# Kernel optimization log

Measured on AMD Instinct MI355X. Metric: run time of the kernel, lower is better.

The kernel has to match this reference:

```python
import jax, jax.numpy as jnp
import numpy as np

B, T, D, H = 32, 512, 512, 8
DH = D // H  # 64


def _pos_enc(t, d):
    # pos / 10000^(2i/d) for ALL i, then sin on even cols, cos on odd cols, scaled by sqrt(d)
    pos = np.arange(t, dtype=np.float64)[:, None]
    i = np.arange(d, dtype=np.float64)[None, :]
    ang = pos / np.power(10000.0, 2.0 * i / d)
    pe = np.empty((t, d), dtype=np.float64)
    pe[:, 0::2] = np.sin(ang[:, 0::2])
    pe[:, 1::2] = np.cos(ang[:, 1::2])
    return jnp.asarray(pe * np.sqrt(float(d)), dtype=jnp.float32)


def setup_inputs() -> dict:
    key = jax.random.key(0)
    ks = jax.random.split(key, 9)
    return {
        "queries": jax.random.normal(ks[0], (B, T, D), dtype=jnp.float32),
        "keys": jax.random.normal(ks[1], (B, T, D), dtype=jnp.float32),
        "query_masks": jax.random.randint(ks[2], (B,), 0, T, dtype=jnp.int32),
        "key_masks": jax.random.randint(ks[3], (B,), 0, T, dtype=jnp.int32),
        "W_Q": jax.random.normal(ks[4], (D, D), dtype=jnp.float32) * 0.05,
        "W_K": jax.random.normal(ks[5], (D, D), dtype=jnp.float32) * 0.05,
        "W_V": jax.random.normal(ks[6], (D, D), dtype=jnp.float32) * 0.05,
        "fw1": jax.random.normal(ks[7], (D, 4 * D), dtype=jnp.float32) * 0.05,
        "fw2": jax.random.normal(ks[8], (4 * D, D), dtype=jnp.float32) * 0.05,
    }


def reference(queries, keys, query_masks, key_masks, W_Q, W_K, W_V, fw1, fw2):
    pe = _pos_enc(T, D)  # [T, D]
    # Source bug kept: queries = posenc(queries); keys = posenc(queries)  -> keys input unused
    q1 = queries + pe[None]          # [B,T,D]
    k1 = q1 + pe[None]               # pos-encoded twice
    Q = q1 @ W_Q                     # [B,T,D]
    Kp = k1 @ W_K                    # [B,T,D]
    V = Kp @ W_V                     # source bug kept: values from projected keys
    # split heads (head-major fold in the original concat(split) idiom)
    Qh = Q.reshape(B, T, H, DH).transpose(2, 0, 1, 3)   # [H,B,T,dh]
    Kh = Kp.reshape(B, T, H, DH).transpose(2, 0, 1, 3)
    Vh = V.reshape(B, T, H, DH).transpose(2, 0, 1, 3)
    scores = jnp.einsum('hbqd,hbkd->hbqk', Qh, Kh) / jnp.sqrt(jnp.float32(DH))
    # source subtracts max over the QUERY axis (axis=1 of [H*B,T,T]) = axis 2 here
    scores = scores - scores.max(axis=2, keepdims=True)
    attn = jax.nn.softmax(scores, axis=-1)
    qmask = (jnp.arange(T)[None, :] < query_masks[:, None]).astype(jnp.float32)  # [B,T]
    attn = attn * qmask[None, :, :, None]
    out = jnp.einsum('hbqk,hbkd->hbqd', attn, Vh)       # [H,B,T,dh]
    result = out.transpose(1, 2, 0, 3).reshape(B, T, D) + q1  # residual with pos-encoded queries
    hidden = jax.nn.relu(result @ fw1)                  # [B,T,4D]
    result = result + hidden @ fw2                      # residual; no layer norm (use_layer_norm=False)
    return result
```

## Files before the change

### kernel.cpp

```cpp
#include <hip/hip_runtime.h>
#include <cstdint>
#include <cstddef>

typedef __bf16 bf16x8 __attribute__((ext_vector_type(8)));
typedef float f32x4 __attribute__((ext_vector_type(4)));
using u16 = unsigned short;
using u32 = unsigned int;

__device__ __forceinline__ u16 f2b(float f) {
  u32 u = __float_as_uint(f);
  u32 r = u + 0x7FFFu + ((u >> 16) & 1u);
  return (u16)(r >> 16);
}
__device__ __forceinline__ float b2f(u16 h) { return __uint_as_float((u32)h << 16); }

__device__ __forceinline__ void gload16(const void* g, void* l) {
  __builtin_amdgcn_global_load_lds((const __attribute__((address_space(1))) void*)g,
                                   (__attribute__((address_space(3))) void*)l, 16, 0, 0);
}

__device__ __forceinline__ u32 mapf(float f) {
  u32 u = __float_as_uint(f);
  return (u & 0x80000000u) ? ~u : (u | 0x80000000u);
}
__device__ __forceinline__ float unmapf(u32 k) {
  u32 u = (k & 0x80000000u) ? (k ^ 0x80000000u) : ~k;
  return __uint_as_float(u);
}
__device__ __forceinline__ u32 cvtpk(float lo, float hi) {
  u32 r;
  asm("v_cvt_pk_bf16_f32 %0, %1, %2" : "=v"(r) : "v"(lo), "v"(hi));
  return r;
}

__device__ __forceinline__ void xcd_swizzle(int& bx, int& by) {
  const int gx = gridDim.x;
  const int nwg = gx * gridDim.y;
  int n = blockIdx.y * gx + blockIdx.x;
  const int cpx = nwg >> 3;
  n = (n & 7) * cpx + (n >> 3);
  bx = n % gx;
  by = n / gx;
}

#define MFMA __builtin_amdgcn_mfma_f32_16x16x32_bf16

__global__ void pe_kernel(float* __restrict__ pe) {
  int i = blockIdx.x * 256 + threadIdx.x;
  if (i >= 512 * 512) return;
  int t = i >> 9, d = i & 511;
  double ang = (double)t * exp((double)d * (-2.0 / 512.0) * log(10000.0));
  double v = (d & 1) ? cos(ang) : sin(ang);
  pe[i] = (float)(v * 22.627416997969522);
}

__global__ void wconv_kernel(const float* __restrict__ WQ, const float* __restrict__ WK,
                             const float* __restrict__ WV, const float* __restrict__ f1,
                             const float* __restrict__ f2,
                             u16* __restrict__ WQth, u16* __restrict__ WQtl,
                             u16* __restrict__ WKth, u16* __restrict__ WKtl,
                             u16* __restrict__ WKb, u16* __restrict__ WVt,
                             u16* __restrict__ f1t, u16* __restrict__ f2t) {
  int i = blockIdx.x * 256 + threadIdx.x;
  if (i < 262144) {
    int n = i >> 9, k = i & 511;
    float wq = WQ[k * 512 + n];
    u16 h = f2b(wq);
    WQth[i] = h;
    WQtl[i] = f2b(wq - b2f(h));
    float wk = WK[k * 512 + n];
    h = f2b(wk);
    WKth[i] = h;
    WKtl[i] = f2b(wk - b2f(h));
    WKb[i] = f2b(WK[i]);
    WVt[i] = f2b(WV[k * 512 + n]);
  } else if (i < 262144 + 1048576) {
    int i2 = i - 262144;
    int n = i2 >> 9, k = i2 & 511;
    f1t[i2] = f2b(f1[k * 2048 + n]);
  } else if (i < 262144 + 2097152) {
    int i3 = i - 262144 - 1048576;
    int n = i3 >> 11, k = i3 & 2047;
    f2t[i3] = f2b(f2[k * 512 + n]);
  }
}

__global__ void prep_kernel(const float* __restrict__ q, const float* __restrict__ pe,
                            u16* __restrict__ q1h, u16* __restrict__ q1l,
                            u16* __restrict__ k1h, u16* __restrict__ k1l) {
  int i4 = blockIdx.x * 256 + threadIdx.x;
  if (i4 >= 2097152) return;
  int i = i4 * 4;
  int td = i & (262144 - 1);
  float4 qv = *(const float4*)&q[i];
  float4 pv = *(const float4*)&pe[td];
  float q1[4] = {qv.x + pv.x, qv.y + pv.y, qv.z + pv.z, qv.w + pv.w};
  float pp[4] = {pv.x, pv.y, pv.z, pv.w};
  ushort4 qh4, ql4, kh4, kl4;
  u16* qhp = (u16*)&qh4;
  u16* qlp = (u16*)&ql4;
  u16* khp = (u16*)&kh4;
  u16* klp = (u16*)&kl4;
#pragma unroll
  for (int j = 0; j < 4; ++j) {
    float k1 = q1[j] + pp[j];
    u16 h = f2b(q1[j]);
    qhp[j] = h;
    qlp[j] = f2b(q1[j] - b2f(h));
    h = f2b(k1);
    khp[j] = h;
    klp[j] = f2b(k1 - b2f(h));
  }
  *(ushort4*)&q1h[i] = qh4;
  *(ushort4*)&q1l[i] = ql4;
  *(ushort4*)&k1h[i] = kh4;
  *(ushort4*)&k1l[i] = kl4;
}

#define GM_BF16 0
#define GM_RELU 2
#define GM_ADDF32 3

template <int MODE>
__global__ __launch_bounds__(256, 3) void gemm_bt(const u16* __restrict__ A,
                                                  const u16* __restrict__ B, int M, int N, int K,
                                                  u16* __restrict__ outb, float* __restrict__ outf,
                                                  const float* __restrict__ res) {
  __shared__ u16 As[128 * 32];
  __shared__ u16 Bs[128 * 32];
  int bxi, byi;
  xcd_swizzle(bxi, byi);
  const int tid = threadIdx.x, lane = tid & 63, w = tid >> 6;
  const int wm = w >> 1, wn = w & 1;
  const long aBase = (long)bxi * 128;
  const long bBase = (long)byi * 128;
  f32x4 acc[4][4] = {};
  const int nk = K >> 5;
  for (int kt = 0; kt < nk; ++kt) {
#pragma unroll
    for (int i = 0; i < 2; ++i) {
      const int c = w * 2 + i;
      const int off = c * 1024 + lane * 16;
      const int r = off >> 6, cb = off & 63;
      gload16((const char*)A + ((aBase + r) * (long)K + (long)kt * 32) * 2 + cb,
              (char*)As + c * 1024);
      gload16((const char*)B + ((bBase + r) * (long)K + (long)kt * 32) * 2 + cb,
              (char*)Bs + c * 1024);
    }
    __syncthreads();
    bf16x8 af[4], bfr[4];
#pragma unroll
    for (int x = 0; x < 4; ++x) {
      af[x] = *(const bf16x8*)&As[(wm * 64 + x * 16 + (lane & 15)) * 32 + (lane >> 4) * 8];
      bfr[x] = *(const bf16x8*)&Bs[(wn * 64 + x * 16 + (lane & 15)) * 32 + (lane >> 4) * 8];
    }
#pragma unroll
    for (int mf = 0; mf < 4; ++mf)
#pragma unroll
      for (int nf = 0; nf < 4; ++nf)
        acc[mf][nf] = MFMA(af[mf], bfr[nf], acc[mf][nf], 0, 0, 0);
    __syncthreads();
  }
#pragma unroll
  for (int mf = 0; mf < 4; ++mf)
#pragma unroll
    for (int nf = 0; nf < 4; ++nf) {
      const long row0 = aBase + wm * 64 + mf * 16 + (lane >> 4) * 4;
      const long col = bBase + wn * 64 + nf * 16 + (lane & 15);
#pragma unroll
      for (int j = 0; j < 4; ++j) {
        float v = acc[mf][nf][j];
        const long row = row0 + j;
        if constexpr (MODE == GM_BF16)
          outb[row * N + col] = f2b(v);
        else if constexpr (MODE == GM_RELU)
          outb[row * N + col] = f2b(v > 0.f ? v : 0.f);
        else
          outf[row * N + col] = res[row * N + col] + v;
      }
    }
}

__global__ __launch_bounds__(256, 3) void gemm_split(const u16* __restrict__ Ah,
                                                     const u16* __restrict__ Al,
                                                     const u16* __restrict__ Bh,
                                                     const u16* __restrict__ Bl, int M, int N,
                                                     int K, u16* __restrict__ Oh,
                                                     u16* __restrict__ Ol) {
  __shared__ u16 Ash[4096], Asl[4096], Bsh[4096], Bsl[4096];
  int bxi, byi;
  xcd_swizzle(bxi, byi);
  const int tid = threadIdx.x, lane = tid & 63, w = tid >> 6;
  const int wm = w >> 1, wn = w & 1;
  const long aBase = (long)bxi * 128;
  const long bBase = (long)byi * 128;
  f32x4 acc[4][4] = {};
  const int nk = K >> 5;
  for (int kt = 0; kt < nk; ++kt) {
#pragma unroll
    for (int i = 0; i < 2; ++i) {
      const int c = w * 2 + i;
      const int off = c * 1024 + lane * 16;
      const int r = off >> 6, cb = off & 63;
      long ga = ((aBase + r) * (long)K + (long)kt * 32) * 2 + cb;
      long gb = ((bBase + r) * (long)K + (long)kt * 32) * 2 + cb;
      gload16((const char*)Ah + ga, (char*)Ash + c * 1024);
      gload16((const char*)Al + ga, (char*)Asl + c * 1024);
      gload16((const char*)Bh + gb, (char*)Bsh + c * 1024);
      gload16((const char*)Bl + gb, (char*)Bsl + c * 1024);
    }
    __syncthreads();
    bf16x8 ah[4], al[4], bh[4], bl[4];
#pragma unroll
    for (int x = 0; x < 4; ++x) {
      int ao = (wm * 64 + x * 16 + (lane & 15)) * 32 + (lane >> 4) * 8;
      int bo = (wn * 64 + x * 16 + (lane & 15)) * 32 + (lane >> 4) * 8;
      ah[x] = *(const bf16x8*)&Ash[ao];
      al[x] = *(const bf16x8*)&Asl[ao];
      bh[x] = *(const bf16x8*)&Bsh[bo];
      bl[x] = *(const bf16x8*)&Bsl[bo];
    }
#pragma unroll
    for (int mf = 0; mf < 4; ++mf)
#pragma unroll
      for (int nf = 0; nf < 4; ++nf) {
        acc[mf][nf] = MFMA(ah[mf], bh[nf], acc[mf][nf], 0, 0, 0);
        acc[mf][nf] = MFMA(ah[mf], bl[nf], acc[mf][nf], 0, 0, 0);
        acc[mf][nf] = MFMA(al[mf], bh[nf], acc[mf][nf], 0, 0, 0);
      }
    __syncthreads();
  }
#pragma unroll
  for (int mf = 0; mf < 4; ++mf)
#pragma unroll
    for (int nf = 0; nf < 4; ++nf) {
      const long row0 = aBase + wm * 64 + mf * 16 + (lane >> 4) * 4;
      const long col = bBase + wn * 64 + nf * 16 + (lane & 15);
#pragma unroll
      for (int j = 0; j < 4; ++j) {
        float v = acc[mf][nf][j];
        const long row = row0 + j;
        u16 h = f2b(v);
        Oh[row * N + col] = h;
        Ol[row * N + col] = f2b(v - b2f(h));
      }
    }
}

__global__ __launch_bounds__(512) void attn_fused(
    const u16* __restrict__ Qh, const u16* __restrict__ Ql, const u16* __restrict__ Kh,
    const u16* __restrict__ Kl, const u16* __restrict__ Vt, const int* __restrict__ qmask,
    const u16* __restrict__ r1h, const u16* __restrict__ r1l, float* __restrict__ resf,
    u16* __restrict__ resb) {
  extern __shared__ char smem[];
  u16* Khi = (u16*)smem;
  u16* Klo = (u16*)(smem + 65536);
  u32* mloc = (u32*)(smem + 131072);
  float* mksf = (float*)(smem + 131072);
  const int tid = threadIdx.x, lane = tid & 63, w = tid >> 6;
  const int qll = lane & 15, g = lane >> 4;
  const int hb = blockIdx.x, b = hb >> 3, h = hb & 7;
  const int qm = qmask[b];
  mloc[tid] = 0u;
  const int srccb = 16 * ((lane & 7) ^ ((lane >> 3) & 7));
#pragma unroll
  for (int c = 0; c < 8; ++c) {
    long gb = ((long)(b * 512 + c * 64 + w * 8 + (lane >> 3)) * 512 + h * 64) * 2 + srccb;
    gload16((const char*)Kh + gb, (char*)Khi + c * 8192 + w * 1024);
    gload16((const char*)Kl + gb, (char*)Klo + c * 8192 + w * 1024);
  }
  bf16x8 qfh[4][2], qfl[4][2];
#pragma unroll
  for (int s = 0; s < 4; ++s) {
    const long qr = (long)(b * 512 + w * 64 + s * 16 + qll) * 512 + h * 64 + g * 8;
    qfh[s][0] = *(const bf16x8*)&Qh[qr];
    qfh[s][1] = *(const bf16x8*)&Qh[qr + 32];
    qfl[s][0] = *(const bf16x8*)&Ql[qr];
    qfl[s][1] = *(const bf16x8*)&Ql[qr + 32];
  }
  __syncthreads();
  const int sw0 = 8 * (g ^ (qll & 7));
  const int sw1 = 8 * ((4 + g) ^ (qll & 7));
  for (int kc = 0; kc < 8; ++kc) {
    const int cb = kc * 4096;
    __builtin_amdgcn_s_setprio(1);
#pragma unroll
    for (int kt = 0; kt < 4; ++kt) {
      const int ko = cb + (kt * 16 + qll) * 64;
      bf16x8 kh0 = *(const bf16x8*)&Khi[ko + sw0];
      bf16x8 kl0 = *(const bf16x8*)&Klo[ko + sw0];
      bf16x8 kh1 = *(const bf16x8*)&Khi[ko + sw1];
      bf16x8 kl1 = *(const bf16x8*)&Klo[ko + sw1];
      float vmax = -3.0e38f;
#pragma unroll
      for (int s = 0; s < 4; ++s) {
        f32x4 acc = {0.f, 0.f, 0.f, 0.f};
        acc = MFMA(qfh[s][0], kh0, acc, 0, 0, 0);
        acc = MFMA(qfh[s][0], kl0, acc, 0, 0, 0);
        acc = MFMA(qfl[s][0], kh0, acc, 0, 0, 0);
        acc = MFMA(qfh[s][1], kh1, acc, 0, 0, 0);
        acc = MFMA(qfh[s][1], kl1, acc, 0, 0, 0);
        acc = MFMA(qfl[s][1], kh1, acc, 0, 0, 0);
        vmax = fmaxf(vmax, fmaxf(fmaxf(acc[0], acc[1]), fmaxf(acc[2], acc[3])));
      }
      vmax = fmaxf(vmax, __shfl_xor(vmax, 16));
      vmax = fmaxf(vmax, __shfl_xor(vmax, 32));
      if (lane < 16) atomicMax(&mloc[kc * 64 + kt * 16 + qll], mapf(vmax));
    }
    __builtin_amdgcn_s_setprio(0);
  }
  __syncthreads();
  float mv = 0.125f * unmapf(mloc[tid]);
  __syncthreads();
  mksf[tid] = mv;
  __syncthreads();
  const u16* vb = Vt + (long)(h * 64) * 16384 + b * 512;
  const int src0 = (g & 1) * 32 + qll;
  const int src1 = src0 + 16;
  const bool lowh = g < 2;
  for (int h2 = 0; h2 < 2; ++h2) {
    bf16x8 sqh[2][2], sql[2][2];
#pragma unroll
    for (int s = 0; s < 2; ++s) {
      const long qr = (long)(b * 512 + w * 64 + (h2 * 2 + s) * 16 + qll) * 512 + h * 64 + g * 8;
      sqh[s][0] = *(const bf16x8*)&Qh[qr];
      sqh[s][1] = *(const bf16x8*)&Qh[qr + 32];
      sql[s][0] = *(const bf16x8*)&Ql[qr];
      sql[s][1] = *(const bf16x8*)&Ql[qr + 32];
    }
    f32x4 o[2][4] = {};
    float mr[2] = {-3.0e38f, -3.0e38f};
    float rsum[2] = {0.f, 0.f};
    for (int kc = 0; kc < 8; ++kc) {
      bf16x8 vf[2][4];
#pragma unroll
      for (int k2 = 0; k2 < 2; ++k2)
#pragma unroll
        for (int nf = 0; nf < 4; ++nf)
          vf[k2][nf] =
              *(const bf16x8*)&vb[(long)(nf * 16 + qll) * 16384 + (kc * 2 + k2) * 32 + g * 8];
      const int cb = kc * 4096;
      f32x4 s4[2][4] = {};
      __builtin_amdgcn_s_setprio(1);
#pragma unroll
      for (int kt = 0; kt < 4; ++kt) {
        const int ko = cb + (kt * 16 + qll) * 64;
        bf16x8 kh0 = *(const bf16x8*)&Khi[ko + sw0];
        bf16x8 kl0 = *(const bf16x8*)&Klo[ko + sw0];
        bf16x8 kh1 = *(const bf16x8*)&Khi[ko + sw1];
        bf16x8 kl1 = *(const bf16x8*)&Klo[ko + sw1];
#pragma unroll
        for (int s = 0; s < 2; ++s) {
          s4[s][kt] = MFMA(kh0, sqh[s][0], s4[s][kt], 0, 0, 0);
          s4[s][kt] = MFMA(kh0, sql[s][0], s4[s][kt], 0, 0, 0);
          s4[s][kt] = MFMA(kl0, sqh[s][0], s4[s][kt], 0, 0, 0);
          s4[s][kt] = MFMA(kh1, sqh[s][1], s4[s][kt], 0, 0, 0);
          s4[s][kt] = MFMA(kh1, sql[s][1], s4[s][kt], 0, 0, 0);
          s4[s][kt] = MFMA(kl1, sqh[s][1], s4[s][kt], 0, 0, 0);
        }
      }
      __builtin_amdgcn_s_setprio(0);
#pragma unroll
      for (int s = 0; s < 2; ++s) {
        float pm = mr[s];
#pragma unroll
        for (int kt = 0; kt < 4; ++kt) {
          f32x4 mrow = *(const f32x4*)&mksf[kc * 64 + kt * 16 + g * 4];
#pragma unroll
          for (int j = 0; j < 4; ++j) {
            float z = s4[s][kt][j] * 0.125f - mrow[j];
            s4[s][kt][j] = z;
            pm = fmaxf(pm, z);
          }
        }
        pm = fmaxf(pm, __shfl_xor(pm, 16));
        pm = fmaxf(pm, __shfl_xor(pm, 32));
        const float f = __expf(mr[s] - pm);
        mr[s] = pm;
        rsum[s] *= f;
#pragma unroll
        for (int nf = 0; nf < 4; ++nf) {
          o[s][nf][0] *= f;
          o[s][nf][1] *= f;
          o[s][nf][2] *= f;
          o[s][nf][3] *= f;
        }
        u32 pk0[4], pk1[4];
#pragma unroll
        for (int kt = 0; kt < 4; ++kt) {
          float p0 = __expf(s4[s][kt][0] - pm);
          float p1 = __expf(s4[s][kt][1] - pm);
          float p2 = __expf(s4[s][kt][2] - pm);
          float p3 = __expf(s4[s][kt][3] - pm);
          rsum[s] += (p0 + p1) + (p2 + p3);
          pk0[kt] = cvtpk(p0, p1);
          pk1[kt] = cvtpk(p2, p3);
        }
        __builtin_amdgcn_s_setprio(1);
#pragma unroll
        for (int k2 = 0; k2 < 2; ++k2) {
          const int fA = 2 * k2, fB = 2 * k2 + 1;
          u32 a00 = __shfl(pk0[fA], src0), b00 = __shfl(pk0[fB], src0);
          u32 a10 = __shfl(pk1[fA], src0), b10 = __shfl(pk1[fB], src0);
          u32 a01 = __shfl(pk0[fA], src1), b01 = __shfl(pk0[fB], src1);
          u32 a11 = __shfl(pk1[fA], src1), b11 = __shfl(pk1[fB], src1);
          union {
            u32 u[4];
            bf16x8 v;
          } pf;
          pf.u[0] = lowh ? a00 : b00;
          pf.u[1] = lowh ? a10 : b10;
          pf.u[2] = lowh ? a01 : b01;
          pf.u[3] = lowh ? a11 : b11;
#pragma unroll
          for (int nf = 0; nf < 4; ++nf) o[s][nf] = MFMA(vf[k2][nf], pf.v, o[s][nf], 0, 0, 0);
        }
        __builtin_amdgcn_s_setprio(0);
      }
    }
#pragma unroll
    for (int s = 0; s < 2; ++s) {
      rsum[s] += __shfl_xor(rsum[s], 16);
      rsum[s] += __shfl_xor(rsum[s], 32);
      const int qg = w * 64 + (h2 * 2 + s) * 16 + qll;
      const float sc = (qg < qm) ? (1.0f / rsum[s]) : 0.0f;
#pragma unroll
      for (int nf = 0; nf < 4; ++nf) {
        const int col = h * 64 + nf * 16 + g * 4;
        const long idx = (long)(b * 512 + qg) * 512 + col;
        ushort4 qh4 = *(const ushort4*)&r1h[idx];
        ushort4 ql4 = *(const ushort4*)&r1l[idx];
        float v0 = o[s][nf][0] * sc + b2f(qh4.x) + b2f(ql4.x);
        float v1 = o[s][nf][1] * sc + b2f(qh4.y) + b2f(ql4.y);
        float v2 = o[s][nf][2] * sc + b2f(qh4.z) + b2f(ql4.z);
        float v3 = o[s][nf][3] * sc + b2f(qh4.w) + b2f(ql4.w);
        *(float4*)&resf[idx] = make_float4(v0, v1, v2, v3);
        ushort4 rb = {f2b(v0), f2b(v1), f2b(v2), f2b(v3)};
        *(ushort4*)&resb[idx] = rb;
      }
    }
  }
}

extern "C" void kernel_launch(void* const* d_in, const int* in_sizes, int n_in, void* d_out,
                              int out_size, void* d_ws, size_t ws_size, hipStream_t stream) {
  (void)in_sizes;
  (void)n_in;
  (void)out_size;
  (void)ws_size;
  const float* queries = (const float*)d_in[0];
  const int* qmask = (const int*)d_in[2];
  const float* WQ = (const float*)d_in[4];
  const float* WK = (const float*)d_in[5];
  const float* WV = (const float*)d_in[6];
  const float* f1 = (const float*)d_in[7];
  const float* f2 = (const float*)d_in[8];
  float* out = (float*)d_out;
  char* ws = (char*)d_ws;
  const size_t A = 16777216;
  u16* q1h = (u16*)(ws + 0 * A);
  u16* q1l = (u16*)(ws + 1 * A);
  u16* k1h = (u16*)(ws + 2 * A);
  u16* k1l = (u16*)(ws + 3 * A);
  u16* Qh = (u16*)(ws + 4 * A);
  u16* Ql = (u16*)(ws + 5 * A);
  u16* Kh = (u16*)(ws + 6 * A);
  u16* Kl = (u16*)(ws + 7 * A);
  u16* Vt = (u16*)(ws + 8 * A);
  u16* resb = (u16*)(ws + 9 * A);
  u16* hid = (u16*)(ws + 0 * A);
  float* pe = (float*)(ws + 10 * A);
  char* wbase = ws + 10 * A + 1572864;
  u16* WQth = (u16*)(wbase + 0 * 524288);
  u16* WQtl = (u16*)(wbase + 1 * 524288);
  u16* WKth = (u16*)(wbase + 2 * 524288);
  u16* WKtl = (u16*)(wbase + 3 * 524288);
  u16* WKb = (u16*)(wbase + 4 * 524288);
  u16* WVt_w = (u16*)(wbase + 5 * 524288);
  u16* WKVt = (u16*)(wbase + 6 * 524288);
  u16* f1t = (u16*)(wbase + 7 * 524288);
  u16* f2t = (u16*)(wbase + 7 * 524288 + 2097152);

  pe_kernel<<<1024, 256, 0, stream>>>(pe);
  wconv_kernel<<<9216, 256, 0, stream>>>(WQ, WK, WV, f1, f2, WQth, WQtl, WKth, WKtl, WKb, WVt_w,
                                         f1t, f2t);
  prep_kernel<<<8192, 256, 0, stream>>>(queries, pe, q1h, q1l, k1h, k1l);
  gemm_bt<GM_BF16><<<dim3(4, 4), 256, 0, stream>>>(WVt_w, WKb, 512, 512, 512, WKVt, nullptr,
                                                   nullptr);
  gemm_split<<<dim3(128, 4), 256, 0, stream>>>(q1h, q1l, WQth, WQtl, 16384, 512, 512, Qh, Ql);
  gemm_split<<<dim3(128, 4), 256, 0, stream>>>(k1h, k1l, WKth, WKtl, 16384, 512, 512, Kh, Kl);
  gemm_bt<GM_BF16><<<dim3(4, 128), 256, 0, stream>>>(WKVt, k1h, 512, 16384, 512, Vt, nullptr,
                                                     nullptr);
  hipFuncSetAttribute((const void*)attn_fused, hipFuncAttributeMaxDynamicSharedMemorySize, 133120);
  attn_fused<<<256, 512, 133120, stream>>>(Qh, Ql, Kh, Kl, Vt, qmask, q1h, q1l, out, resb);
  gemm_bt<GM_RELU><<<dim3(128, 16), 256, 0, stream>>>(resb, f1t, 16384, 2048, 512, hid, nullptr,
                                                      nullptr);
  gemm_bt<GM_ADDF32><<<dim3(128, 4), 256, 0, stream>>>(hid, f2t, 16384, 512, 2048, nullptr, out,
                                                       out);
}
```

Before: 328.2 us.

## Use LDS-tiled transpose kernels for weight conversion and drop XCD swizzle

Replaces the single strided-gather weight conversion kernel with per-matrix 64x64 LDS-tiled transpose-and-convert kernels plus a plain vectorised convert for WK, giving coalesced reads and writes. Also removes the XCD block-index swizzle from both GEMM kernels so blocks map directly to tiles. The cost is more kernel launches, and losing the swizzle may change L2 locality across XCDs.

```diff
diff --git a/kernel.cpp b/kernel.cpp
--- a/kernel.cpp
+++ b/kernel.cpp
@@ -31,16 +31,6 @@
   u32 r;
   asm("v_cvt_pk_bf16_f32 %0, %1, %2" : "=v"(r) : "v"(lo), "v"(hi));
   return r;
-}
-
-__device__ __forceinline__ void xcd_swizzle(int& bx, int& by) {
-  const int gx = gridDim.x;
-  const int nwg = gx * gridDim.y;
-  int n = blockIdx.y * gx + blockIdx.x;
-  const int cpx = nwg >> 3;
-  n = (n & 7) * cpx + (n >> 3);
-  bx = n % gx;
-  by = n / gx;
 }
 
 #define MFMA __builtin_amdgcn_mfma_f32_16x16x32_bf16
@@ -54,35 +44,49 @@
   pe[i] = (float)(v * 22.627416997969522);
 }
 
-__global__ void wconv_kernel(const float* __restrict__ WQ, const float* __restrict__ WK,
-                             const float* __restrict__ WV, const float* __restrict__ f1,
-                             const float* __restrict__ f2,
-                             u16* __restrict__ WQth, u16* __restrict__ WQtl,
-                             u16* __restrict__ WKth, u16* __restrict__ WKtl,
-                             u16* __restrict__ WKb, u16* __restrict__ WVt,
-                             u16* __restrict__ f1t, u16* __restrict__ f2t) {
-  int i = blockIdx.x * 256 + threadIdx.x;
-  if (i < 262144) {
-    int n = i >> 9, k = i & 511;
-    float wq = WQ[k * 512 + n];
-    u16 h = f2b(wq);
-    WQth[i] = h;
-    WQtl[i] = f2b(wq - b2f(h));
-    float wk = WK[k * 512 + n];
-    h = f2b(wk);
-    WKth[i] = h;
-    WKtl[i] = f2b(wk - b2f(h));
-    WKb[i] = f2b(WK[i]);
-    WVt[i] = f2b(WV[k * 512 + n]);
-  } else if (i < 262144 + 1048576) {
-    int i2 = i - 262144;
-    int n = i2 >> 9, k = i2 & 511;
-    f1t[i2] = f2b(f1[k * 2048 + n]);
-  } else if (i < 262144 + 2097152) {
-    int i3 = i - 262144 - 1048576;
-    int n = i3 >> 11, k = i3 & 2047;
-    f2t[i3] = f2b(f2[k * 512 + n]);
-  }
+template <int SPLIT>
+__global__ __launch_bounds__(256) void tconv_kernel(const float* __restrict__ in, int R, int C,
+                                                    u16* __restrict__ outh,
+                                                    u16* __restrict__ outl) {
+  __shared__ float tile[64][65];
+  const int t = threadIdx.x;
+  const long r0 = (long)blockIdx.x * 64, c0 = (long)blockIdx.y * 64;
+#pragma unroll
+  for (int it = 0; it < 4; ++it) {
+    int r = it * 16 + (t >> 4);
+    int c = (t & 15) * 4;
+    float4 v = *(const float4*)&in[(r0 + r) * C + c0 + c];
+    tile[r][c] = v.x;
+    tile[r][c + 1] = v.y;
+    tile[r][c + 2] = v.z;
+    tile[r][c + 3] = v.w;
+  }
+  __syncthreads();
+#pragma unroll
+  for (int it = 0; it < 4; ++it) {
+    int oc = it * 16 + (t >> 4);
+    int orr = (t & 15) * 4;
+    ushort4 h4, l4;
+    u16* hp = (u16*)&h4;
+    u16* lp = (u16*)&l4;
+#pragma unroll
+    for (int j = 0; j < 4; ++j) {
+      float v = tile[orr + j][oc];
+      u16 h = f2b(v);
+      hp[j] = h;
+      if (SPLIT) lp[j] = f2b(v - b2f(h));
+    }
+    *(ushort4*)&outh[(c0 + oc) * R + r0 + orr] = h4;
+    if (SPLIT) *(ushort4*)&outl[(c0 + oc) * R + r0 + orr] = l4;
+  }
+}
+
+__global__ void conv_kernel(const float* __restrict__ in, u16* __restrict__ out, int n4) {
+  int i4 = blockIdx.x * 256 + threadIdx.x;
+  if (i4 >= n4) return;
+  float4 v = *(const float4*)&in[i4 * 4];
+  ushort4 o = {f2b(v.x), f2b(v.y), f2b(v.z), f2b(v.w)};
+  *(ushort4*)&out[i4 * 4] = o;
 }
 
 __global__ void prep_kernel(const float* __restrict__ q, const float* __restrict__ pe,
@@ -128,12 +132,10 @@
                                                   const float* __restrict__ res) {
   __shared__ u16 As[128 * 32];
   __shared__ u16 Bs[128 * 32];
-  int bxi, byi;
-  xcd_swizzle(bxi, byi);
   const int tid = threadIdx.x, lane = tid & 63, w = tid >> 6;
   const int wm = w >> 1, wn = w & 1;
-  const long aBase = (long)bxi * 128;
-  const long bBase = (long)byi * 128;
+  const long aBase = (long)blockIdx.x * 128;
+  const long bBase = (long)blockIdx.y * 128;
   f32x4 acc[4][4] = {};
   const int nk = K >> 5;
   for (int kt = 0; kt < nk; ++kt) {
@@ -188,12 +190,10 @@
                                                      int K, u16* __restrict__ Oh,
                                                      u16* __restrict__ Ol) {
   __shared__ u16 Ash[4096], Asl[4096], Bsh[4096], Bsl[4096];
-  int bxi, byi;
-  xcd_swizzle(bxi, byi);
   const int tid = threadIdx.x, lane = tid & 63, w = tid >> 6;
   const int wm = w >> 1, wn = w & 1;
-  const long aBase = (long)bxi * 128;
-  const long bBase = (long)byi * 128;
+  const long aBase = (long)blockIdx.x * 128;
+  const long bBase = (long)blockIdx.y * 128;
   f32x4 acc[4][4] = {};
   const int nk = K >> 5;
   for (int kt = 0; kt < nk; ++kt) {
@@ -482,8 +482,12 @@
   u16* f2t = (u16*)(wbase + 7 * 524288 + 2097152);
 
   pe_kernel<<<1024, 256, 0, stream>>>(pe);
-  wconv_kernel<<<9216, 256, 0, stream>>>(WQ, WK, WV, f1, f2, WQth, WQtl, WKth, WKtl, WKb, WVt_w,
-                                         f1t, f2t);
+  tconv_kernel<1><<<dim3(8, 8), 256, 0, stream>>>(WQ, 512, 512, WQth, WQtl);
+  tconv_kernel<1><<<dim3(8, 8), 256, 0, stream>>>(WK, 512, 512, WKth, WKtl);
+  tconv_kernel<0><<<dim3(8, 8), 256, 0, stream>>>(WV, 512, 512, WVt_w, nullptr);
+  tconv_kernel<0><<<dim3(8, 32), 256, 0, stream>>>(f1, 512, 2048, f1t, nullptr);
+  tconv_kernel<0><<<dim3(32, 8), 256, 0, stream>>>(f2, 2048, 512, f2t, nullptr);
+  conv_kernel<<<256, 256, 0, stream>>>(WK, WKb, 65536);
   prep_kernel<<<8192, 256, 0, stream>>>(queries, pe, q1h, q1l, k1h, k1l);
   gemm_bt<GM_BF16><<<dim3(4, 4), 256, 0, stream>>>(WVt_w, WKb, 512, 512, 512, WKVt, nullptr,
                                                    nullptr);
```

Measured after the change: 313.8 us. -4.4%, faster.
